# Optimization experiments

Measured on AMD Instinct MI355X. Metric: run time of the kernel, lower is better.

The kernel has to match this reference:

```python
import jax, jax.numpy as jnp
import numpy as np

UNITS = 128
ATT_UNITS = 64
NUM_HEADS = 8


def setup_inputs() -> dict:
    key = jax.random.key(0)
    ks = jax.random.split(key, 8)
    N, F, E = 50000, 128, 800000
    x = jax.random.normal(ks[0], (N, F), dtype=jnp.float32)
    edge_index = jax.random.randint(ks[1], (2, E), 0, N, dtype=jnp.int32)
    glorot = lambda k, shp: jax.random.uniform(k, shp, jnp.float32,
                                               -jnp.sqrt(6.0 / (shp[0] + shp[1])),
                                               jnp.sqrt(6.0 / (shp[0] + shp[1])))
    return {
        "x": x,
        "edge_index": edge_index,
        "query_kernel": glorot(ks[2], (F, ATT_UNITS)),
        "query_bias": jnp.zeros((ATT_UNITS,), jnp.float32),
        "key_kernel": glorot(ks[3], (F, ATT_UNITS)),
        "key_bias": jnp.zeros((ATT_UNITS,), jnp.float32),
        "kernel": glorot(ks[4], (F, UNITS)),
        "bias": jnp.zeros((UNITS,), jnp.float32),
    }


def reference(x, edge_index, query_kernel, query_bias, key_kernel, key_bias, kernel, bias):
    N = x.shape[0]
    H = NUM_HEADS
    # add self-loop edges (tf_geometric add_self_loop_edge)
    loop = jnp.arange(N, dtype=edge_index.dtype)
    row = jnp.concatenate([edge_index[0], loop])  # target nodes
    col = jnp.concatenate([edge_index[1], loop])  # source nodes
    E = row.shape[0]

    Q = jax.nn.relu(x @ query_kernel + query_bias)[row]  # [E, A]
    K = jax.nn.relu(x @ key_kernel + key_bias)[col]      # [E, A]
    V = (x @ kernel)[col]                                # [E, U]

    # split feature dim into contiguous head chunks (matches tf.split)
    Qh = Q.reshape(E, H, -1)
    Kh = K.reshape(E, H, -1)
    Vh = V.reshape(E, H, -1)

    score = jnp.sum(Qh * Kh, axis=-1)  # [E, H]
    # segment softmax over edges grouped by target node (row)
    smax = jax.ops.segment_max(score, row, num_segments=N)  # [N, H]
    ex = jnp.exp(score - smax[row])
    ssum = jax.ops.segment_sum(ex, row, num_segments=N)     # [N, H]
    alpha = ex / ssum[row]                                  # [E, H]

    agg = jax.ops.segment_sum(Vh * alpha[..., None], row, num_segments=N)  # [N, H, U/H]
    h = agg.reshape(N, -1) + bias
    return h
```

## Files before the change

### kernel.cpp

```cpp
#include <hip/hip_runtime.h>

#define SHIFT 10.0f
#define CAP 64
#define NXCD 8
#define BSH 7
#define CAPB 3072

typedef __attribute__((ext_vector_type(8))) short bf16x8;
typedef __attribute__((ext_vector_type(4))) float f32x4;

__device__ inline uint16_t bf16r(float f) {
    uint32_t u = __float_as_uint(f);
    return (uint16_t)((u + 0x7FFFu + ((u >> 16) & 1u)) >> 16);
}
__device__ inline float bf2f(uint16_t h) {
    return __uint_as_float(((uint32_t)h) << 16);
}
__device__ inline uint32_t pack_bf16x2(float lo, float hi) {
    return (uint32_t)bf16r(lo) | ((uint32_t)bf16r(hi) << 16);
}

#define ABSZ 512
#define AEPT 8
#define PREP_BLKS 32
__global__ __launch_bounds__(ABSZ) void prep_bin(
    const float* __restrict__ Wq, const float* __restrict__ Wk,
    const float* __restrict__ Wv, uint32_t* __restrict__ Wh32,
    uint32_t* __restrict__ Wl32,
    const int* __restrict__ row, const int* __restrict__ col,
    int* __restrict__ bucketCursor, uint32_t* __restrict__ inter, int E)
{
    if (blockIdx.x < PREP_BLKS) {
        int t = blockIdx.x * ABSZ + threadIdx.x;
        int c = t >> 6;
        int k2 = t & 63;
        float f0, f1;
        if (c < 64)       { f0 = Wq[(2 * k2) * 64 + c];          f1 = Wq[(2 * k2 + 1) * 64 + c]; }
        else if (c < 128) { f0 = Wk[(2 * k2) * 64 + (c - 64)];   f1 = Wk[(2 * k2 + 1) * 64 + (c - 64)]; }
        else              { f0 = Wv[(2 * k2) * 128 + (c - 128)]; f1 = Wv[(2 * k2 + 1) * 128 + (c - 128)]; }
        uint16_t h0 = bf16r(f0), h1 = bf16r(f1);
        uint16_t l0 = bf16r(f0 - bf2f(h0)), l1 = bf16r(f1 - bf2f(h1));
        Wh32[t] = (uint32_t)h0 | ((uint32_t)h1 << 16);
        Wl32[t] = (uint32_t)l0 | ((uint32_t)l1 << 16);
        return;
    }

    __shared__ int hist[512];
    __shared__ int basebuf[512];
    const int t = threadIdx.x;
    hist[t] = 0;
    __syncthreads();

    const int base0 = (blockIdx.x - PREP_BLKS) * ABSZ * AEPT;
    uint32_t pk[AEPT];
    int dg[AEPT], rk[AEPT];
#pragma unroll
    for (int k = 0; k < AEPT; ++k) {
        int e = base0 + k * ABSZ + t;
        if (e < E) {
            int r = row[e];
            int c = col[e];
            pk[k] = ((uint32_t)r << 16) | (uint32_t)c;
            dg[k] = r >> BSH;
            rk[k] = atomicAdd(&hist[dg[k]], 1);
        } else dg[k] = -1;
    }
    __syncthreads();

    {
        int h = hist[t];
        basebuf[t] = h ? atomicAdd(&bucketCursor[t], h) : 0;
    }
    __syncthreads();

#pragma unroll
    for (int k = 0; k < AEPT; ++k) {
        if (dg[k] >= 0) {
            int idx = basebuf[dg[k]] + rk[k];
            if (idx < CAPB)
                inter[(size_t)dg[k] * CAPB + idx] = pk[k];
        }
    }
}

__global__ __launch_bounds__(256) void fused_nlb(
    const uint32_t* __restrict__ inter, const int* __restrict__ bucketCursor,
    uint16_t* __restrict__ csr, int* __restrict__ deg,
    const float* __restrict__ x,
    const uint16_t* __restrict__ Wh, const uint16_t* __restrict__ Wl,
    const float* __restrict__ bq, const float* __restrict__ bk,
    float* __restrict__ Qn, uint32_t* __restrict__ Kh, uint32_t* __restrict__ Vh,
    int N, int NB)
{
    __shared__ uint16_t Ah[64][136];
    __shared__ uint16_t Al[64][136];
    __shared__ int cnt[128];

    if (blockIdx.x < NB) {
        const int b = blockIdx.x;
        const int t = threadIdx.x;
        if (t < 128) cnt[t] = 0;
        __syncthreads();

        const int count = min(bucketCursor[b], CAPB);
        const uint32_t* src = inter + (size_t)b * CAPB;
        for (int i = t; i < count; i += 256) {
            uint32_t u = src[i];
            int r = (int)(u >> 16);
            int pos = atomicAdd(&cnt[r & 127], 1);
            if (pos < CAP - 1)
                csr[(size_t)r * CAP + pos] = (uint16_t)(u & 0xFFFFu);
        }
        __syncthreads();

        const int node = (b << BSH) + t;
        if (t < 128 && node < N) deg[node] = min(cnt[t], CAP - 1);
        return;
    }

    const int tid = threadIdx.x;
    const int lane = tid & 63;
    const int wv = tid >> 6;
    const int block0 = (blockIdx.x - NB) * 64;
    if (block0 >= N) return;

    float4 v[8];
#pragma unroll
    for (int i = 0; i < 8; ++i) {
        int idx = tid + i * 256;
        int node = idx >> 5;
        int c4 = idx & 31;
        v[i] = make_float4(0.f, 0.f, 0.f, 0.f);
        if (block0 + node < N)
            v[i] = reinterpret_cast<const float4*>(x + (size_t)(block0 + node) * 128)[c4];
    }
#pragma unroll
    for (int i = 0; i < 8; ++i) {
        int idx = tid + i * 256;
        int node = idx >> 5;
        int c4 = idx & 31;
        uint16_t hx = bf16r(v[i].x), hy = bf16r(v[i].y), hz = bf16r(v[i].z), hw = bf16r(v[i].w);
        uint2 uh, ul;
        uh.x = (uint32_t)hx | ((uint32_t)hy << 16);
        uh.y = (uint32_t)hz | ((uint32_t)hw << 16);
        ul.x = (uint32_t)bf16r(v[i].x - bf2f(hx)) | ((uint32_t)bf16r(v[i].y - bf2f(hy)) << 16);
        ul.y = (uint32_t)bf16r(v[i].z - bf2f(hz)) | ((uint32_t)bf16r(v[i].w - bf2f(hw)) << 16);
        *reinterpret_cast<uint2*>(&Ah[node][c4 * 4]) = uh;
        *reinterpret_cast<uint2*>(&Al[node][c4 * 4]) = ul;
    }
    __syncthreads();

    f32x4 acc[4][4] = {};
#pragma unroll
    for (int ks = 0; ks < 4; ++ks) {
        bf16x8 bh[4], bl[4];
#pragma unroll
        for (int cf = 0; cf < 4; ++cf) {
            size_t off = (size_t)(wv * 64 + cf * 16 + (lane & 15)) * 128
                         + ks * 32 + (lane >> 4) * 8;
            bh[cf] = *reinterpret_cast<const bf16x8*>(Wh + off);
            bl[cf] = *reinterpret_cast<const bf16x8*>(Wl + off);
        }
#pragma unroll
        for (int rf = 0; rf < 4; ++rf) {
            bf16x8 ah = *reinterpret_cast<const bf16x8*>(
                &Ah[rf * 16 + (lane & 15)][ks * 32 + (lane >> 4) * 8]);
            bf16x8 al = *reinterpret_cast<const bf16x8*>(
                &Al[rf * 16 + (lane & 15)][ks * 32 + (lane >> 4) * 8]);
#pragma unroll
            for (int cf = 0; cf < 4; ++cf)
                acc[rf][cf] = __builtin_amdgcn_mfma_f32_16x16x32_bf16(
                    ah, bh[cf], acc[rf][cf], 0, 0, 0);
#pragma unroll
            for (int cf = 0; cf < 4; ++cf)
                acc[rf][cf] = __builtin_amdgcn_mfma_f32_16x16x32_bf16(
                    ah, bl[cf], acc[rf][cf], 0, 0, 0);
#pragma unroll
            for (int cf = 0; cf < 4; ++cf)
                acc[rf][cf] = __builtin_amdgcn_mfma_f32_16x16x32_bf16(
                    al, bh[cf], acc[rf][cf], 0, 0, 0);
        }
    }

#pragma unroll
    for (int rf = 0; rf < 4; ++rf) {
#pragma unroll
        for (int cf = 0; cf < 4; ++cf) {
            const int ocol = wv * 64 + cf * 16 + (lane & 15);
#pragma unroll
            for (int r = 0; r < 4; ++r) {
                const int orow = rf * 16 + (lane >> 4) * 4 + r;
                const int node = block0 + orow;
                float v2 = acc[rf][cf][r];
                if (wv == 0) {
                    v2 = fmaxf(v2 + bq[ocol], 0.f);
                    if (node < N) Qn[(size_t)node * 64 + ocol] = v2;
                } else if (wv == 1) {
                    const int ck = ocol - 64;
                    v2 = fmaxf(v2 + bk[ck], 0.f);
                    float vp = __shfl_xor(v2, 1);
                    if (node < N && !(lane & 1))
                        Kh[(size_t)node * 32 + (ck >> 1)] = pack_bf16x2(v2, vp);
                } else {
                    const int cv = ocol - 128;
                    float vp = __shfl_xor(v2, 1);
                    if (node < N && !(lane & 1))
                        Vh[(size_t)node * 64 + (cv >> 1)] = pack_bf16x2(v2, vp);
                }
            }
        }
    }
}

__device__ inline float dot2bf(uint32_t u, float q0, float q1) {
    return __uint_as_float(u << 16) * q0 + __uint_as_float(u & 0xFFFF0000u) * q1;
}

__global__ __launch_bounds__(256) void agg5(
    const int* __restrict__ deg_, const uint16_t* __restrict__ csr,
    const float* __restrict__ Qn, const uint32_t* __restrict__ Kh,
    const uint32_t* __restrict__ Vh, const float* __restrict__ bias,
    float* __restrict__ out, int N)
{
    __shared__ float qs[4][64];
    __shared__ float es[4][8][36];
    __shared__ int   cis[4][32];

    const int wv = threadIdx.x >> 6;
    const int lane = threadIdx.x & 63;

    const int xcd = blockIdx.x & (NXCD - 1);
    const int nslice = (N + NXCD - 1) / NXCD;
    const int ln = (blockIdx.x >> 3) * 4 + wv;
    if (ln >= nslice) return;
    const int n = xcd * nslice + ln;
    if (n >= N) return;

    const int deg = min(deg_[n], CAP - 1);
    const int tot = deg + 1;

    qs[wv][lane] = Qn[(size_t)n * 64 + lane];
    __builtin_amdgcn_wave_barrier();

    const int e2 = lane >> 1;
    const int half = lane & 1;
    const int h2 = lane >> 3;
    const float* esrow = &es[wv][h2][0];

    float accx = 0.f, accy = 0.f, accL = 0.f;

    for (int base = 0; base < tot; base += 32) {
        const int nn = min(32, tot - base);
        const int idxe = base + e2;
        const bool valide = (idxe < tot);
        int c = n;
        if (valide && idxe < deg) c = (int)csr[(size_t)n * CAP + idxe];
        if (!valide) c = 0;
        cis[wv][e2] = c;

        const uint4* Krow = reinterpret_cast<const uint4*>(Kh + (size_t)c * 32 + half * 16);
        const float* qh = &qs[wv][half * 32];
#pragma unroll
        for (int hh = 0; hh < 4; ++hh) {
            uint4 kv = Krow[hh];
            const float* q8 = qh + hh * 8;
            float s;
            s  = dot2bf(kv.x, q8[0], q8[1]);
            s += dot2bf(kv.y, q8[2], q8[3]);
            s += dot2bf(kv.z, q8[4], q8[5]);
            s += dot2bf(kv.w, q8[6], q8[7]);
            es[wv][half * 4 + hh][e2] = valide ? __expf(s - SHIFT) : 0.f;
        }
        __builtin_amdgcn_wave_barrier();

        const int nn4 = (nn + 3) & ~3;
        for (int i = 0; i < nn4; i += 4) {
            int4 c4 = *reinterpret_cast<const int4*>(&cis[wv][i]);
            float4 e4 = *reinterpret_cast<const float4*>(&esrow[i]);
            uint32_t u0 = Vh[(size_t)c4.x * 64 + lane];
            uint32_t u1 = Vh[(size_t)c4.y * 64 + lane];
            uint32_t u2 = Vh[(size_t)c4.z * 64 + lane];
            uint32_t u3 = Vh[(size_t)c4.w * 64 + lane];
            accx += e4.x * __uint_as_float(u0 << 16);
            accy += e4.x * __uint_as_float(u0 & 0xFFFF0000u);
            accL += e4.x;
            accx += e4.y * __uint_as_float(u1 << 16);
            accy += e4.y * __uint_as_float(u1 & 0xFFFF0000u);
            accL += e4.y;
            accx += e4.z * __uint_as_float(u2 << 16);
            accy += e4.z * __uint_as_float(u2 & 0xFFFF0000u);
            accL += e4.z;
            accx += e4.w * __uint_as_float(u3 << 16);
            accy += e4.w * __uint_as_float(u3 & 0xFFFF0000u);
            accL += e4.w;
        }
        __builtin_amdgcn_wave_barrier();
    }

    float2 b = reinterpret_cast<const float2*>(bias)[lane];
    float inv = 1.0f / accL;
    float2 o;
    o.x = accx * inv + b.x;
    o.y = accy * inv + b.y;
    reinterpret_cast<float2*>(out)[(size_t)n * 64 + lane] = o;
}

extern "C" void kernel_launch(void* const* d_in, const int* in_sizes, int n_in,
                              void* d_out, int out_size, void* d_ws, size_t ws_size,
                              hipStream_t stream) {
    const float* x    = (const float*)d_in[0];
    const int*   ei   = (const int*)d_in[1];
    const float* Wq   = (const float*)d_in[2];
    const float* bq   = (const float*)d_in[3];
    const float* Wk   = (const float*)d_in[4];
    const float* bk   = (const float*)d_in[5];
    const float* Wv   = (const float*)d_in[6];
    const float* bias = (const float*)d_in[7];
    float* out = (float*)d_out;

    const int N = in_sizes[0] / 128;
    const int E = in_sizes[1] / 2;
    const int* row = ei;
    const int* col = ei + E;
    const int NB = (N + (1 << BSH) - 1) >> BSH;

    float*    Qn     = (float*)d_ws;
    uint32_t* Kh     = (uint32_t*)(Qn + (size_t)N * 64);
    uint32_t* Vh     = Kh + (size_t)N * 32;
    uint32_t* Wh32   = Vh + (size_t)N * 64;
    uint32_t* Wl32   = Wh32 + 16384;
    int*      deg    = (int*)(Wl32 + 16384);
    int*      bcur   = deg + N;
    uint32_t* inter  = (uint32_t*)(bcur + 512);
    uint16_t* csr    = (uint16_t*)(inter + (size_t)NB * CAPB);

    const int nslice = (N + NXCD - 1) / NXCD;
    const int agg_grid = ((nslice + 3) / 4) * NXCD;
    const int nl_grid = (N + 63) / 64;
    const int binA_grid = (E + ABSZ * AEPT - 1) / (ABSZ * AEPT);

    hipMemsetAsync(bcur, 0, 512 * sizeof(int), stream);
    prep_bin<<<PREP_BLKS + binA_grid, ABSZ, 0, stream>>>(
        Wq, Wk, Wv, Wh32, Wl32, row, col, bcur, inter, E);
    fused_nlb<<<NB + nl_grid, 256, 0, stream>>>(
        inter, bcur, csr, deg,
        x, (const uint16_t*)Wh32, (const uint16_t*)Wl32, bq, bk,
        Qn, Kh, Vh, N, NB);
    agg5<<<agg_grid, 256, 0, stream>>>(
        deg, csr, Qn, Kh, Vh, bias, out, N);
}
```

Before: 106.1 us.

## Regroup kernels: fuse edge binning with node linear, split bucket scatter out

Replaces the memset plus combined weight-prep/binning kernel with a small weight-prep kernel that also zeroes the bucket cursors. Edge binning (first pass) now runs in the same launch as the node projection GEMM, and the per-bucket CSR scatter becomes its own kernel. Binning blocks use 256 threads with 16 edges per thread. The goal is to overlap the memory-bound binning with the compute-heavy projection and drop the memset launch, at the cost of one extra kernel launch and higher register pressure in the binning blocks.

```diff
diff --git a/kernel.cpp b/kernel.cpp
--- a/kernel.cpp
+++ b/kernel.cpp
@@ -20,108 +20,85 @@
     return (uint32_t)bf16r(lo) | ((uint32_t)bf16r(hi) << 16);
 }
 
-#define ABSZ 512
-#define AEPT 8
-#define PREP_BLKS 32
-__global__ __launch_bounds__(ABSZ) void prep_bin(
+__global__ __launch_bounds__(256) void prep_w(
     const float* __restrict__ Wq, const float* __restrict__ Wk,
     const float* __restrict__ Wv, uint32_t* __restrict__ Wh32,
-    uint32_t* __restrict__ Wl32,
+    uint32_t* __restrict__ Wl32, int* __restrict__ bucketCursor)
+{
+    int t = blockIdx.x * 256 + threadIdx.x;
+    if (t < 512) bucketCursor[t] = 0;
+    if (t >= 256 * 64) return;
+    int c = t >> 6;
+    int k2 = t & 63;
+    float f0, f1;
+    if (c < 64)       { f0 = Wq[(2 * k2) * 64 + c];          f1 = Wq[(2 * k2 + 1) * 64 + c]; }
+    else if (c < 128) { f0 = Wk[(2 * k2) * 64 + (c - 64)];   f1 = Wk[(2 * k2 + 1) * 64 + (c - 64)]; }
+    else              { f0 = Wv[(2 * k2) * 128 + (c - 128)]; f1 = Wv[(2 * k2 + 1) * 128 + (c - 128)]; }
+    uint16_t h0 = bf16r(f0), h1 = bf16r(f1);
+    uint16_t l0 = bf16r(f0 - bf2f(h0)), l1 = bf16r(f1 - bf2f(h1));
+    Wh32[t] = (uint32_t)h0 | ((uint32_t)h1 << 16);
+    Wl32[t] = (uint32_t)l0 | ((uint32_t)l1 << 16);
+}
+
+#define AEPT 16
+__global__ __launch_bounds__(256) void bin_nl(
     const int* __restrict__ row, const int* __restrict__ col,
-    int* __restrict__ bucketCursor, uint32_t* __restrict__ inter, int E)
-{
-    if (blockIdx.x < PREP_BLKS) {
-        int t = blockIdx.x * ABSZ + threadIdx.x;
-        int c = t >> 6;
-        int k2 = t & 63;
-        float f0, f1;
-        if (c < 64)       { f0 = Wq[(2 * k2) * 64 + c];          f1 = Wq[(2 * k2 + 1) * 64 + c]; }
-        else if (c < 128) { f0 = Wk[(2 * k2) * 64 + (c - 64)];   f1 = Wk[(2 * k2 + 1) * 64 + (c - 64)]; }
-        else              { f0 = Wv[(2 * k2) * 128 + (c - 128)]; f1 = Wv[(2 * k2 + 1) * 128 + (c - 128)]; }
-        uint16_t h0 = bf16r(f0), h1 = bf16r(f1);
-        uint16_t l0 = bf16r(f0 - bf2f(h0)), l1 = bf16r(f1 - bf2f(h1));
-        Wh32[t] = (uint32_t)h0 | ((uint32_t)h1 << 16);
-        Wl32[t] = (uint32_t)l0 | ((uint32_t)l1 << 16);
-        return;
-    }
-
-    __shared__ int hist[512];
-    __shared__ int basebuf[512];
-    const int t = threadIdx.x;
-    hist[t] = 0;
-    __syncthreads();
-
-    const int base0 = (blockIdx.x - PREP_BLKS) * ABSZ * AEPT;
-    uint32_t pk[AEPT];
-    int dg[AEPT], rk[AEPT];
-#pragma unroll
-    for (int k = 0; k < AEPT; ++k) {
-        int e = base0 + k * ABSZ + t;
-        if (e < E) {
-            int r = row[e];
-            int c = col[e];
-            pk[k] = ((uint32_t)r << 16) | (uint32_t)c;
-            dg[k] = r >> BSH;
-            rk[k] = atomicAdd(&hist[dg[k]], 1);
-        } else dg[k] = -1;
-    }
-    __syncthreads();
-
-    {
-        int h = hist[t];
-        basebuf[t] = h ? atomicAdd(&bucketCursor[t], h) : 0;
-    }
-    __syncthreads();
-
-#pragma unroll
-    for (int k = 0; k < AEPT; ++k) {
-        if (dg[k] >= 0) {
-            int idx = basebuf[dg[k]] + rk[k];
-            if (idx < CAPB)
-                inter[(size_t)dg[k] * CAPB + idx] = pk[k];
-        }
-    }
-}
-
-__global__ __launch_bounds__(256) void fused_nlb(
-    const uint32_t* __restrict__ inter, const int* __restrict__ bucketCursor,
-    uint16_t* __restrict__ csr, int* __restrict__ deg,
+    int* __restrict__ bucketCursor, uint32_t* __restrict__ inter, int E,
     const float* __restrict__ x,
     const uint16_t* __restrict__ Wh, const uint16_t* __restrict__ Wl,
     const float* __restrict__ bq, const float* __restrict__ bk,
     float* __restrict__ Qn, uint32_t* __restrict__ Kh, uint32_t* __restrict__ Vh,
-    int N, int NB)
+    int N, int BINA)
 {
     __shared__ uint16_t Ah[64][136];
     __shared__ uint16_t Al[64][136];
-    __shared__ int cnt[128];
-
-    if (blockIdx.x < NB) {
-        const int b = blockIdx.x;
+    __shared__ int hist[512];
+    __shared__ int basebuf[512];
+
+    if (blockIdx.x < BINA) {
         const int t = threadIdx.x;
-        if (t < 128) cnt[t] = 0;
+        hist[t] = 0; hist[t + 256] = 0;
         __syncthreads();
 
-        const int count = min(bucketCursor[b], CAPB);
-        const uint32_t* src = inter + (size_t)b * CAPB;
-        for (int i = t; i < count; i += 256) {
-            uint32_t u = src[i];
-            int r = (int)(u >> 16);
-            int pos = atomicAdd(&cnt[r & 127], 1);
-            if (pos < CAP - 1)
-                csr[(size_t)r * CAP + pos] = (uint16_t)(u & 0xFFFFu);
+        const int base0 = blockIdx.x * 256 * AEPT;
+        uint32_t pk[AEPT];
+        int dg[AEPT], rk[AEPT];
+#pragma unroll
+        for (int k = 0; k < AEPT; ++k) {
+            int e = base0 + k * 256 + t;
+            if (e < E) {
+                int r = row[e];
+                int c = col[e];
+                pk[k] = ((uint32_t)r << 16) | (uint32_t)c;
+                dg[k] = r >> BSH;
+                rk[k] = atomicAdd(&hist[dg[k]], 1);
+            } else dg[k] = -1;
         }
         __syncthreads();
 
-        const int node = (b << BSH) + t;
-        if (t < 128 && node < N) deg[node] = min(cnt[t], CAP - 1);
+#pragma unroll
+        for (int b2 = 0; b2 < 2; ++b2) {
+            int i = t + b2 * 256;
+            int h = hist[i];
+            basebuf[i] = h ? atomicAdd(&bucketCursor[i], h) : 0;
+        }
+        __syncthreads();
+
+#pragma unroll
+        for (int k = 0; k < AEPT; ++k) {
+            if (dg[k] >= 0) {
+                int idx = basebuf[dg[k]] + rk[k];
+                if (idx < CAPB)
+                    inter[(size_t)dg[k] * CAPB + idx] = pk[k];
+            }
+        }
         return;
     }
 
     const int tid = threadIdx.x;
     const int lane = tid & 63;
     const int wv = tid >> 6;
-    const int block0 = (blockIdx.x - NB) * 64;
+    const int block0 = (blockIdx.x - BINA) * 64;
     if (block0 >= N) return;
 
     float4 v[8];
@@ -212,6 +189,31 @@
     }
 }
 
+__global__ __launch_bounds__(256) void bin_b(
+    const uint32_t* __restrict__ inter, const int* __restrict__ bucketCursor,
+    uint16_t* __restrict__ csr, int* __restrict__ deg, int N)
+{
+    __shared__ int cnt[128];
+    const int b = blockIdx.x;
+    const int t = threadIdx.x;
+    if (t < 128) cnt[t] = 0;
+    __syncthreads();
+
+    const int count = min(bucketCursor[b], CAPB);
+    const uint32_t* src = inter + (size_t)b * CAPB;
+    for (int i = t; i < count; i += 256) {
+        uint32_t u = src[i];
+        int r = (int)(u >> 16);
+        int pos = atomicAdd(&cnt[r & 127], 1);
+        if (pos < CAP - 1)
+            csr[(size_t)r * CAP + pos] = (uint16_t)(u & 0xFFFFu);
+    }
+    __syncthreads();
+
+    const int node = (b << BSH) + t;
+    if (t < 128 && node < N) deg[node] = min(cnt[t], CAP - 1);
+}
+
 __device__ inline float dot2bf(uint32_t u, float q0, float q1) {
     return __uint_as_float(u << 16) * q0 + __uint_as_float(u & 0xFFFF0000u) * q1;
 }
@@ -337,15 +339,14 @@
     const int nslice = (N + NXCD - 1) / NXCD;
     const int agg_grid = ((nslice + 3) / 4) * NXCD;
     const int nl_grid = (N + 63) / 64;
-    const int binA_grid = (E + ABSZ * AEPT - 1) / (ABSZ * AEPT);
-
-    hipMemsetAsync(bcur, 0, 512 * sizeof(int), stream);
-    prep_bin<<<PREP_BLKS + binA_grid, ABSZ, 0, stream>>>(
-        Wq, Wk, Wv, Wh32, Wl32, row, col, bcur, inter, E);
-    fused_nlb<<<NB + nl_grid, 256, 0, stream>>>(
-        inter, bcur, csr, deg,
+    const int binA_grid = (E + 256 * AEPT - 1) / (256 * AEPT);
+
+    prep_w<<<64, 256, 0, stream>>>(Wq, Wk, Wv, Wh32, Wl32, bcur);
+    bin_nl<<<binA_grid + nl_grid, 256, 0, stream>>>(
+        row, col, bcur, inter, E,
         x, (const uint16_t*)Wh32, (const uint16_t*)Wl32, bq, bk,
-        Qn, Kh, Vh, N, NB);
+        Qn, Kh, Vh, N, binA_grid);
+    bin_b<<<NB, 256, 0, stream>>>(inter, bcur, csr, deg, N);
     agg5<<<agg_grid, 256, 0, stream>>>(
         deg, csr, Qn, Kh, Vh, bias, out, N);
 }
```

Result: slower. 109.6 us (+3.3%).
